# Performance work log

Measured on AMD Instinct MI355X. Metric: run time of the kernel, lower is better.

## Reference

```python
import jax, jax.numpy as jnp
import numpy as np

_DN = ('NCHW', 'OIHW', 'NCHW')

def _conv(x, w, stride=1, pad=1, dil=1, groups=1):
    return jax.lax.conv_general_dilated(
        x, w, window_strides=(stride, stride),
        padding=[(pad, pad), (pad, pad)],
        rhs_dilation=(dil, dil),
        feature_group_count=groups,
        dimension_numbers=_DN)


def setup_inputs() -> dict:
    key = jax.random.key(0)
    k1, k2, k3 = jax.random.split(key, 3)
    B, T, C_in, H, W = 4, 16, 32, 64, 64
    hidden = 64
    x = jax.random.normal(k1, (B, T, C_in, H, W), dtype=jnp.float32)
    # input-to-hidden conv weight: 3 gates stacked along out channels
    fan_i = C_in * 3 * 3
    W_i = jax.random.normal(k2, (3 * hidden, C_in, 3, 3), dtype=jnp.float32) / np.sqrt(fan_i)
    fan_h = hidden * 3 * 3
    W_h = jax.random.normal(k3, (3 * hidden, hidden, 3, 3), dtype=jnp.float32) / np.sqrt(fan_h)
    return {"x": x, "W_i": W_i, "W_h": W_h}


def reference(x, W_i, W_h):
    # x: [B, T, C_in, H, W] (batch_first). Single-layer unidirectional ConvGRU.
    B, T, C_in, H, Wd = x.shape
    hidden = W_h.shape[1]

    def cell(h, x_t):
        gi = _conv(x_t, W_i)          # [B, 3*hidden, H, W]
        gh = _conv(h, W_h)            # [B, 3*hidden, H, W]
        i_r, i_z, i_n = jnp.split(gi, 3, axis=1)
        h_r, h_z, h_n = jnp.split(gh, 3, axis=1)
        r = jax.nn.sigmoid(i_r + h_r)
        z = jax.nn.sigmoid(i_z + h_z)
        n = jnp.tanh(i_n + r * h_n)
        h_new = (1.0 - z) * n + z * h
        return h_new, h_new

    h0 = jnp.zeros((B, hidden, H, Wd), dtype=x.dtype)
    xs = jnp.moveaxis(x, 1, 0)        # [T, B, C_in, H, W]
    _, hs = jax.lax.scan(cell, h0, xs)
    return jnp.moveaxis(hs, 0, 1)     # [B, T, hidden, H, W]
```

## Files before the change

kernel.cpp:

```cpp
#include <hip/hip_runtime.h>
#include <math.h>

constexpr int B_  = 4;
constexpr int T_  = 16;
constexpr int CIN = 32;
constexpr int HID = 64;
constexpr int HH  = 64;
constexpr int WW  = 64;
constexpr int HW  = HH * WW;

constexpr int TR = 8,  TC = 16;
constexpr int PR = TR + 2, PC = TC + 2;
constexpr int CSL = 40;
constexpr int KCH = 32;
constexpr int ASLAB_HW  = 3 * 36 * 16 * 8;
constexpr int ATOTAL    = 12 * ASLAB_HW;
constexpr int TIN_HW    = PR * PC * CSL;
constexpr int TIN_GRAN  = TIN_HW / 8;
constexpr int ROW_HW    = 66 * CSL;
constexpr int PIMG_HW   = 66 * ROW_HW;

constexpr size_t A2_HW    = (size_t)ATOTAL;
constexpr size_t XT_OFF   = A2_HW;
constexpr size_t XT_HW    = (size_t)64 * PIMG_HW;
constexpr size_t HT_OFF   = XT_OFF + XT_HW;
constexpr size_t HTBUF_HW = (size_t)8 * PIMG_HW;
constexpr size_t WS_NEED_BYTES = (A2_HW + XT_HW + 2 * HTBUF_HW) * 2;

typedef __attribute__((ext_vector_type(8))) short bf16x8;
typedef __attribute__((ext_vector_type(4))) float f32x4;

#define GLOAD_LDS16(gsrc, ldst) \
  __builtin_amdgcn_global_load_lds((const __attribute__((address_space(1))) void*)(gsrc), \
                                   (__attribute__((address_space(3))) void*)(ldst), 16, 0, 0)

__device__ inline unsigned short f2bf(float f) {
    union { float f; unsigned u; } v; v.f = f;
    return (unsigned short)((v.u + 0x7FFFu + ((v.u >> 16) & 1u)) >> 16);
}
__device__ inline float bf2f(unsigned short h) {
    union { unsigned u; float f; } v; v.u = (unsigned)h << 16; return v.f;
}

__global__ void wconv(const float* __restrict__ Wi, const float* __restrict__ Wh,
                      unsigned short* __restrict__ A2) {
    int idx = blockIdx.x * 256 + threadIdx.x;
    if (idx >= ATOTAL) return;
    int ic  = idx & 31;
    int r1  = idx >> 5;
    int tap = r1 % 9;
    int r2  = r1 / 9;
    int m   = r2 & 15;
    int r3  = r2 >> 4;
    int gt  = r3 % 3;
    int r4  = r3 / 3;
    int hg  = r4 & 3;
    int ch  = r4 >> 2;
    int o   = gt * 64 + hg * 16 + m;
    float w = (ch == 0) ? Wi[(o * CIN + ic) * 9 + tap]
                        : Wh[(o * HID + (ch - 1) * 32 + ic) * 9 + tap];
    size_t dst = (size_t)(ch * 4 + hg) * ASLAB_HW
               + ((size_t)(gt * 36 + tap * 4 + (ic >> 3)) * 16 + m) * 8 + (ic & 7);
    A2[dst] = f2bf(w);
}

__global__ void xfill(const float* __restrict__ x, unsigned short* __restrict__ xT) {
    const int riT = blockIdx.x;
    const int bt  = blockIdx.y;
    unsigned short* dst = xT + (size_t)bt * PIMG_HW + (size_t)riT * ROW_HW;
    __shared__ float lds[64 * 41];

    const bool interior = (riT >= 1 && riT <= 64);
    if (interior) {
        const float* src = x + (size_t)bt * 32 * HW + (riT - 1) * WW;
        const int p = threadIdx.x & 63;
        #pragma unroll
        for (int j = 0; j < 8; ++j) {
            int c = j * 4 + (threadIdx.x >> 6);
            lds[p * 41 + c] = src[c * HW + p];
        }
    }
    __syncthreads();
    for (int g = threadIdx.x; g < ROW_HW / 8; g += 256) {
        bf16x8 vv;
        #pragma unroll
        for (int k = 0; k < 8; ++k) {
            int off = g * 8 + k;
            int px = off / CSL, slot = off - px * CSL;
            float v = 0.f;
            if (interior && slot < 32 && px >= 1 && px <= 64)
                v = lds[(px - 1) * 41 + slot];
            vv[k] = (short)f2bf(v);
        }
        *(bf16x8*)(dst + g * 8) = vv;
    }
}

__global__ void hzero(unsigned short* __restrict__ hT, int n16) {
    int i = blockIdx.x * 256 + threadIdx.x;
    if (i < n16) ((f32x4*)hT)[i] = f32x4{0.f, 0.f, 0.f, 0.f};
}

__global__ __launch_bounds__(256, 2) void convgru_mfma(
    const unsigned short* __restrict__ xT,
    const unsigned short* __restrict__ A2,
    const unsigned short* __restrict__ hTrd,
    unsigned short* __restrict__ hTwr,
    float* __restrict__ out, int t)
{
    __shared__ __align__(16) unsigned short t0s[TIN_HW];
    __shared__ __align__(16) unsigned short t1s[TIN_HW];
    __shared__ __align__(16) unsigned short t2s[TIN_HW];

    const int tid  = threadIdx.x;
    const int lane = tid & 63, wave = tid >> 6;
    const int px   = lane & 15, kl = lane >> 4;
    const int ty = blockIdx.x >> 2, tx = blockIdx.x & 3;
    const int hg = blockIdx.y, b = blockIdx.z;
    const int gy0 = ty * TR, gx0 = tx * TC;

    const unsigned short* xs = xT + (size_t)(b * T_ + t) * PIMG_HW;
    const int rowbase = gy0 * 66 + gx0;

    f32x4 accR[2] = {}, accZ[2] = {}, accNX[2] = {}, accNH[2] = {};
    bf16x8 a[27];

    auto stage_tin = [&](const unsigned short* src, unsigned short* dst) {
        #pragma unroll
        for (int j = 0; j < 4; ++j) {
            int G = tid + j * 256;
            if (G < TIN_GRAN) {
                int r = G / 90, w = G - 90 * r;
                GLOAD_LDS16(src + (size_t)(rowbase + r * 66) * CSL + w * 8, dst + G * 8);
            }
        }
    };
    auto regA = [&](int ch) {
        const unsigned short* s = A2 + (size_t)(ch * 4 + hg) * ASLAB_HW + lane * 8;
        #pragma unroll
        for (int i = 0; i < 27; ++i)
            a[i] = *(const bf16x8*)(s + (size_t)((i / 9) * 36 + (i % 9) * 4) * 128);
    };

    const int rb = (wave * 2 * PC + px) * CSL + kl * 8;

    auto compute = [&](const unsigned short* tb, bool isX) {
        bf16x8 P[4][3];
        #pragma unroll
        for (int r = 0; r < 4; ++r)
            #pragma unroll
            for (int s = 0; s < 3; ++s)
                P[r][s] = *(const bf16x8*)(tb + rb + (r * PC + s) * CSL);
        #pragma unroll
        for (int dy = 0; dy < 3; ++dy) {
            #pragma unroll
            for (int dx = 0; dx < 3; ++dx) {
                const int tap = dy * 3 + dx;
                bf16x8 b0 = P[dy][dx], b1 = P[dy + 1][dx];
                bf16x8 ar = a[tap], az = a[9 + tap], an = a[18 + tap];
                accR[0] = __builtin_amdgcn_mfma_f32_16x16x32_bf16(ar, b0, accR[0], 0, 0, 0);
                accR[1] = __builtin_amdgcn_mfma_f32_16x16x32_bf16(ar, b1, accR[1], 0, 0, 0);
                accZ[0] = __builtin_amdgcn_mfma_f32_16x16x32_bf16(az, b0, accZ[0], 0, 0, 0);
                accZ[1] = __builtin_amdgcn_mfma_f32_16x16x32_bf16(az, b1, accZ[1], 0, 0, 0);
                if (isX) {
                    accNX[0] = __builtin_amdgcn_mfma_f32_16x16x32_bf16(an, b0, accNX[0], 0, 0, 0);
                    accNX[1] = __builtin_amdgcn_mfma_f32_16x16x32_bf16(an, b1, accNX[1], 0, 0, 0);
                } else {
                    accNH[0] = __builtin_amdgcn_mfma_f32_16x16x32_bf16(an, b0, accNH[0], 0, 0, 0);
                    accNH[1] = __builtin_amdgcn_mfma_f32_16x16x32_bf16(an, b1, accNH[1], 0, 0, 0);
                }
            }
        }
    };

    stage_tin(xs, t0s);
    if (t > 0) {
        stage_tin(hTrd + (size_t)(b * 2 + 0) * PIMG_HW, t1s);
        stage_tin(hTrd + (size_t)(b * 2 + 1) * PIMG_HW, t2s);
    }
    regA(0);
    __syncthreads();
    compute(t0s, true);
    if (t > 0) {
        regA(1);
        compute(t1s, false);
        regA(2);
        compute(t2s, false);
    }

    float* outp = out + ((size_t)(b * T_ + t)) * HID * HW;
    const int c0   = hg * 16 + kl * 4;
    const int slot = c0 & 31;
    const unsigned short* hbuf = (hg < 2) ? t1s : t2s;
    #pragma unroll
    for (int g = 0; g < 2; ++g) {
        int gy = gy0 + wave * 2 + g;
        int gx = gx0 + px;
        float hvf[4] = {0.f, 0.f, 0.f, 0.f};
        if (t > 0) {
            const unsigned short* hp =
                hbuf + ((wave * 2 + g + 1) * PC + (px + 1)) * CSL + slot;
            #pragma unroll
            for (int q = 0; q < 4; ++q) hvf[q] = bf2f(hp[q]);
        }
        unsigned short hvals[4];
        #pragma unroll
        for (int q = 0; q < 4; ++q) {
            int c = c0 + q;
            float sr = __builtin_amdgcn_rcpf(1.f + __expf(-accR[g][q]));
            float sz = __builtin_amdgcn_rcpf(1.f + __expf(-accZ[g][q]));
            float ag = accNX[g][q] + sr * accNH[g][q];
            float nn = 2.f * __builtin_amdgcn_rcpf(1.f + __expf(-2.f * ag)) - 1.f;
            float hn = nn + sz * (hvf[q] - nn);
            outp[(size_t)c * HW + gy * WW + gx] = hn;
            hvals[q] = f2bf(hn);
        }
        unsigned short* hd = hTwr + (size_t)(b * 2 + (c0 >> 5)) * PIMG_HW
                           + (size_t)((gy + 1) * 66 + (gx + 1)) * CSL + slot;
        *(uint2*)hd = *(const uint2*)hvals;
    }
}

constexpr int F_AROWB = 640;
constexpr int R4_ASLAB = 48 * 9 * KCH;
constexpr int R4_AVEC  = R4_ASLAB / 8;
constexpr int R4_ATOT  = 12 * R4_ASLAB;
__global__ void wconv_r4(const float* __restrict__ Wi, const float* __restrict__ Wh,
                         unsigned short* __restrict__ A2) {
    int idx = blockIdx.x * 256 + threadIdx.x;
    if (idx >= R4_ATOT) return;
    int ic = idx & 31; int r1 = idx >> 5;
    int tap = r1 % 9; int r2 = r1 / 9;
    int m = r2 & 15; int r3 = r2 >> 4;
    int gt = r3 % 3; int r4 = r3 / 3;
    int hg = r4 & 3; int ch = r4 >> 2;
    int o = gt * 64 + hg * 16 + m;
    float w = (ch == 0) ? Wi[(o * CIN + ic) * 9 + tap]
                        : Wh[(o * HID + (ch - 1) * 32 + ic) * 9 + tap];
    A2[idx] = f2bf(w);
}
__global__ __launch_bounds__(256, 2) void convgru_r4(
    const float* __restrict__ x, const unsigned short* __restrict__ A2,
    const float* hall, float* out, int t)
{
    __shared__ __align__(16) unsigned short tin[PR * PC * 40];
    __shared__ __align__(16) unsigned short Alr[48 * (F_AROWB / 2)];
    const int tid = threadIdx.x;
    const int lane = tid & 63, wave = tid >> 6;
    const int px = lane & 15, kl = lane >> 4;
    const int ty = blockIdx.x >> 2, tx = blockIdx.x & 3;
    const int hg = blockIdx.y, b = blockIdx.z;
    const int gy0 = ty * TR, gx0 = tx * TC;
    const int nch = (t > 0) ? 3 : 1;
    const float* hb = (t > 0) ? (hall + ((size_t)(b * T_ + t - 1)) * HID * HW) : nullptr;
    const float* xb = x + ((size_t)(b * T_ + t)) * CIN * HW;
    f32x4 accR[2] = {}, accZ[2] = {}, accNX[2] = {}, accNH[2] = {};
    float ireg[23]; bf16x8 areg[7];
    auto load_in = [&](int ch) {
        const float* src = (ch == 0) ? xb : (hb + (size_t)(ch - 1) * KCH * HW);
        #pragma unroll
        for (int j = 0; j < 23; ++j) {
            int e = tid + j * 256; float v = 0.f;
            if (e < PR * PC * KCH) {
                int ic = e / (PR * PC); int rem = e - ic * (PR * PC);
                int r = rem / PC, c = rem - r * PC;
                int gy = gy0 + r - 1, gx = gx0 + c - 1;
                if ((unsigned)gy < (unsigned)HH && (unsigned)gx < (unsigned)WW)
                    v = src[ic * HW + gy * WW + gx];
            }
            ireg[j] = v;
        }
    };
    auto load_Ar = [&](int ch) {
        const unsigned short* s = A2 + (size_t)(ch * 4 + hg) * R4_ASLAB;
        #pragma unroll
        for (int j = 0; j < 7; ++j) { int v = tid + j * 256; if (v < R4_AVEC) areg[j] = *(const bf16x8*)(s + v * 8); }
    };
    auto write_in = [&]() {
        #pragma unroll
        for (int j = 0; j < 23; ++j) {
            int e = tid + j * 256;
            if (e < PR * PC * KCH) {
                int ic = e / (PR * PC); int rem = e - ic * (PR * PC);
                int r = rem / PC, c = rem - r * PC;
                tin[(r * PC + c) * 40 + ic] = f2bf(ireg[j]);
            }
        }
    };
    auto write_Ar = [&]() {
        #pragma unroll
        for (int j = 0; j < 7; ++j) {
            int v = tid + j * 256;
            if (v < R4_AVEC) {
                int row = v / 36; int kb = (v - row * 36) * 16;
                char* dst = (char*)Alr + row * F_AROWB + (kb ^ ((row & 7) << 4));
                *(bf16x8*)dst = areg[j];
            }
        }
    };
    const int rb0 = ((wave * 2 + 0) * PC + px) * 40 + kl * 8;
    const int rb1 = rb0 + PC * 40;
    const int swA = (px & 7) << 4;
    auto compute = [&](bool isX) {
        #pragma unroll
        for (int tap = 0; tap < 9; ++tap) {
            const int dy = tap / 3, dx = tap - 3 * dy;
            const int toff = (dy * PC + dx) * 40;
            bf16x8 b0 = *(const bf16x8*)(tin + rb0 + toff);
            bf16x8 b1 = *(const bf16x8*)(tin + rb1 + toff);
            const char* ab = (const char*)Alr + px * F_AROWB + ((tap * 64 + kl * 16) ^ swA);
            bf16x8 ar = *(const bf16x8*)(ab);
            bf16x8 az = *(const bf16x8*)(ab + 16 * F_AROWB);
            bf16x8 an = *(const bf16x8*)(ab + 32 * F_AROWB);
            accR[0] = __builtin_amdgcn_mfma_f32_16x16x32_bf16(ar, b0, accR[0], 0, 0, 0);
            accR[1] = __builtin_amdgcn_mfma_f32_16x16x32_bf16(ar, b1, accR[1], 0, 0, 0);
            accZ[0] = __builtin_amdgcn_mfma_f32_16x16x32_bf16(az, b0, accZ[0], 0, 0, 0);
            accZ[1] = __builtin_amdgcn_mfma_f32_16x16x32_bf16(az, b1, accZ[1], 0, 0, 0);
            if (isX) {
                accNX[0] = __builtin_amdgcn_mfma_f32_16x16x32_bf16(an, b0, accNX[0], 0, 0, 0);
                accNX[1] = __builtin_amdgcn_mfma_f32_16x16x32_bf16(an, b1, accNX[1], 0, 0, 0);
            } else {
                accNH[0] = __builtin_amdgcn_mfma_f32_16x16x32_bf16(an, b0, accNH[0], 0, 0, 0);
                accNH[1] = __builtin_amdgcn_mfma_f32_16x16x32_bf16(an, b1, accNH[1], 0, 0, 0);
            }
        }
    };
    load_in(0); load_Ar(0); write_in(); write_Ar();
    __syncthreads();
    for (int ch = 0; ch < nch; ++ch) {
        if (ch + 1 < nch) { load_in(ch + 1); load_Ar(ch + 1); }
        compute(ch == 0);
        __syncthreads();
        if (ch + 1 < nch) { write_in(); write_Ar(); __syncthreads(); }
    }
    float* outp = out + ((size_t)(b * T_ + t)) * HID * HW;
    #pragma unroll
    for (int g = 0; g < 2; ++g) {
        int gy = gy0 + wave * 2 + g; int gx = gx0 + px;
        #pragma unroll
        for (int q = 0; q < 4; ++q) {
            int c = hg * 16 + kl * 4 + q;
            float sr = 1.f / (1.f + expf(-accR[g][q]));
            float sz = 1.f / (1.f + expf(-accZ[g][q]));
            float nn = tanhf(accNX[g][q] + sr * accNH[g][q]);
            float hv = hb ? hb[(size_t)c * HW + gy * WW + gx] : 0.f;
            outp[(size_t)c * HW + gy * WW + gx] = (1.f - sz) * nn + sz * hv;
        }
    }
}

extern "C" void kernel_launch(void* const* d_in, const int* in_sizes, int n_in,
                              void* d_out, int out_size, void* d_ws, size_t ws_size,
                              hipStream_t stream) {
    const float* x  = (const float*)d_in[0];
    const float* Wi = (const float*)d_in[1];
    const float* Wh = (const float*)d_in[2];
    float* out = (float*)d_out;

    if (ws_size >= WS_NEED_BYTES) {
        unsigned short* A2  = (unsigned short*)d_ws;
        unsigned short* xT  = A2 + XT_OFF;
        unsigned short* hT0 = A2 + HT_OFF;
        unsigned short* hT1 = hT0 + HTBUF_HW;

        wconv<<<(ATOTAL + 255) / 256, 256, 0, stream>>>(Wi, Wh, A2);
        xfill<<<dim3(66, 64), 256, 0, stream>>>(x, xT);
        {
            int n16 = (int)(2 * HTBUF_HW / 8);
            hzero<<<(n16 + 255) / 256, 256, 0, stream>>>(hT0, n16);
        }
        for (int t = 0; t < T_; ++t) {
            unsigned short* rd = (t & 1) ? hT1 : hT0;
            unsigned short* wr = (t & 1) ? hT0 : hT1;
            convgru_mfma<<<dim3(32, 4, 4), 256, 0, stream>>>(xT, A2, rd, wr, out, t);
        }
    } else {
        unsigned short* A2 = (unsigned short*)d_ws;
        wconv_r4<<<(R4_ATOT + 255) / 256, 256, 0, stream>>>(Wi, Wh, A2);
        for (int t = 0; t < T_; ++t)
            convgru_r4<<<dim3(32, 4, 4), 256, 0, stream>>>(x, A2, out, out, t);
    }
}
```

Before: 174.5 us.

## Merge prep kernels into one launch and prefetch next-channel weights during MFMA

Combines the weight conversion, x repacking and hidden-state zeroing into a single prep kernel that dispatches on block index, removing two kernel launches. Inside the recurrent kernel, the weight registers for the next channel chunk are loaded tap by tap while the current chunk's MFMAs run, instead of a blocking reload between chunks. This hides global weight-load latency but reuses the same register array in place, which could raise register pressure or limit how freely the compiler schedules the loads.

```diff
diff --git a/kernel.cpp b/kernel.cpp
--- a/kernel.cpp
+++ b/kernel.cpp
@@ -27,6 +27,12 @@
 constexpr size_t HTBUF_HW = (size_t)8 * PIMG_HW;
 constexpr size_t WS_NEED_BYTES = (A2_HW + XT_HW + 2 * HTBUF_HW) * 2;
 
+constexpr int PB_XFILL = 66 * 64;
+constexpr int PB_WCONV = (ATOTAL + 255) / 256;
+constexpr int HZ_GRAN  = (int)(2 * HTBUF_HW / 8);
+constexpr int PB_HZERO = (HZ_GRAN + 255) / 256;
+constexpr int PB_TOTAL = PB_XFILL + PB_WCONV + PB_HZERO;
+
 typedef __attribute__((ext_vector_type(8))) short bf16x8;
 typedef __attribute__((ext_vector_type(4))) float f32x4;
 
@@ -42,63 +48,65 @@
     union { unsigned u; float f; } v; v.u = (unsigned)h << 16; return v.f;
 }
 
-__global__ void wconv(const float* __restrict__ Wi, const float* __restrict__ Wh,
-                      unsigned short* __restrict__ A2) {
-    int idx = blockIdx.x * 256 + threadIdx.x;
-    if (idx >= ATOTAL) return;
-    int ic  = idx & 31;
-    int r1  = idx >> 5;
-    int tap = r1 % 9;
-    int r2  = r1 / 9;
-    int m   = r2 & 15;
-    int r3  = r2 >> 4;
-    int gt  = r3 % 3;
-    int r4  = r3 / 3;
-    int hg  = r4 & 3;
-    int ch  = r4 >> 2;
-    int o   = gt * 64 + hg * 16 + m;
-    float w = (ch == 0) ? Wi[(o * CIN + ic) * 9 + tap]
-                        : Wh[(o * HID + (ch - 1) * 32 + ic) * 9 + tap];
-    size_t dst = (size_t)(ch * 4 + hg) * ASLAB_HW
-               + ((size_t)(gt * 36 + tap * 4 + (ic >> 3)) * 16 + m) * 8 + (ic & 7);
-    A2[dst] = f2bf(w);
-}
-
-__global__ void xfill(const float* __restrict__ x, unsigned short* __restrict__ xT) {
-    const int riT = blockIdx.x;
-    const int bt  = blockIdx.y;
-    unsigned short* dst = xT + (size_t)bt * PIMG_HW + (size_t)riT * ROW_HW;
+__global__ void prep(const float* __restrict__ x,
+                     const float* __restrict__ Wi, const float* __restrict__ Wh,
+                     unsigned short* __restrict__ A2,
+                     unsigned short* __restrict__ xT,
+                     unsigned short* __restrict__ hT) {
     __shared__ float lds[64 * 41];
-
-    const bool interior = (riT >= 1 && riT <= 64);
-    if (interior) {
-        const float* src = x + (size_t)bt * 32 * HW + (riT - 1) * WW;
-        const int p = threadIdx.x & 63;
-        #pragma unroll
-        for (int j = 0; j < 8; ++j) {
-            int c = j * 4 + (threadIdx.x >> 6);
-            lds[p * 41 + c] = src[c * HW + p];
-        }
-    }
-    __syncthreads();
-    for (int g = threadIdx.x; g < ROW_HW / 8; g += 256) {
-        bf16x8 vv;
-        #pragma unroll
-        for (int k = 0; k < 8; ++k) {
-            int off = g * 8 + k;
-            int px = off / CSL, slot = off - px * CSL;
-            float v = 0.f;
-            if (interior && slot < 32 && px >= 1 && px <= 64)
-                v = lds[(px - 1) * 41 + slot];
-            vv[k] = (short)f2bf(v);
-        }
-        *(bf16x8*)(dst + g * 8) = vv;
-    }
-}
-
-__global__ void hzero(unsigned short* __restrict__ hT, int n16) {
-    int i = blockIdx.x * 256 + threadIdx.x;
-    if (i < n16) ((f32x4*)hT)[i] = f32x4{0.f, 0.f, 0.f, 0.f};
+    const int bid = blockIdx.x;
+
+    if (bid < PB_XFILL) {
+        const int riT = bid % 66;
+        const int bt  = bid / 66;
+        unsigned short* dst = xT + (size_t)bt * PIMG_HW + (size_t)riT * ROW_HW;
+        const bool interior = (riT >= 1 && riT <= 64);
+        if (interior) {
+            const float* src = x + (size_t)bt * 32 * HW + (riT - 1) * WW;
+            const int p = threadIdx.x & 63;
+            #pragma unroll
+            for (int j = 0; j < 8; ++j) {
+                int c = j * 4 + (threadIdx.x >> 6);
+                lds[p * 41 + c] = src[c * HW + p];
+            }
+        }
+        __syncthreads();
+        for (int g = threadIdx.x; g < ROW_HW / 8; g += 256) {
+            bf16x8 vv;
+            #pragma unroll
+            for (int k = 0; k < 8; ++k) {
+                int off = g * 8 + k;
+                int px = off / CSL, slot = off - px * CSL;
+                float v = 0.f;
+                if (interior && slot < 32 && px >= 1 && px <= 64)
+                    v = lds[(px - 1) * 41 + slot];
+                vv[k] = (short)f2bf(v);
+            }
+            *(bf16x8*)(dst + g * 8) = vv;
+        }
+    } else if (bid < PB_XFILL + PB_WCONV) {
+        int idx = (bid - PB_XFILL) * 256 + threadIdx.x;
+        if (idx >= ATOTAL) return;
+        int ic  = idx & 31;
+        int r1  = idx >> 5;
+        int tap = r1 % 9;
+        int r2  = r1 / 9;
+        int m   = r2 & 15;
+        int r3  = r2 >> 4;
+        int gt  = r3 % 3;
+        int r4  = r3 / 3;
+        int hg  = r4 & 3;
+        int ch  = r4 >> 2;
+        int o   = gt * 64 + hg * 16 + m;
+        float w = (ch == 0) ? Wi[(o * CIN + ic) * 9 + tap]
+                            : Wh[(o * HID + (ch - 1) * 32 + ic) * 9 + tap];
+        size_t dst = (size_t)(ch * 4 + hg) * ASLAB_HW
+                   + ((size_t)(gt * 36 + tap * 4 + (ic >> 3)) * 16 + m) * 8 + (ic & 7);
+        A2[dst] = f2bf(w);
+    } else {
+        int i = (bid - PB_XFILL - PB_WCONV) * 256 + threadIdx.x;
+        if (i < HZ_GRAN) ((f32x4*)hT)[i] = f32x4{0.f, 0.f, 0.f, 0.f};
+    }
 }
 
 __global__ __launch_bounds__(256, 2) void convgru_mfma(
@@ -144,7 +152,7 @@
 
     const int rb = (wave * 2 * PC + px) * CSL + kl * 8;
 
-    auto compute = [&](const unsigned short* tb, bool isX) {
+    auto compute = [&](const unsigned short* tb, bool isX, const unsigned short* nextA) {
         bf16x8 P[4][3];
         #pragma unroll
         for (int r = 0; r < 4; ++r)
@@ -158,6 +166,11 @@
                 const int tap = dy * 3 + dx;
                 bf16x8 b0 = P[dy][dx], b1 = P[dy + 1][dx];
                 bf16x8 ar = a[tap], az = a[9 + tap], an = a[18 + tap];
+                if (nextA) {
+                    a[tap]      = *(const bf16x8*)(nextA + (size_t)(0 * 36 + tap * 4) * 128);
+                    a[9 + tap]  = *(const bf16x8*)(nextA + (size_t)(1 * 36 + tap * 4) * 128);
+                    a[18 + tap] = *(const bf16x8*)(nextA + (size_t)(2 * 36 + tap * 4) * 128);
+                }
                 accR[0] = __builtin_amdgcn_mfma_f32_16x16x32_bf16(ar, b0, accR[0], 0, 0, 0);
                 accR[1] = __builtin_amdgcn_mfma_f32_16x16x32_bf16(ar, b1, accR[1], 0, 0, 0);
                 accZ[0] = __builtin_amdgcn_mfma_f32_16x16x32_bf16(az, b0, accZ[0], 0, 0, 0);
@@ -180,12 +193,16 @@
     }
     regA(0);
     __syncthreads();
-    compute(t0s, true);
+
+    const unsigned short* A1p = (t > 0)
+        ? A2 + (size_t)(1 * 4 + hg) * ASLAB_HW + lane * 8 : nullptr;
+    const unsigned short* A2p = (t > 0)
+        ? A2 + (size_t)(2 * 4 + hg) * ASLAB_HW + lane * 8 : nullptr;
+
+    compute(t0s, true, A1p);
     if (t > 0) {
-        regA(1);
-        compute(t1s, false);
-        regA(2);
-        compute(t2s, false);
+        compute(t1s, false, A2p);
+        compute(t2s, false, nullptr);
     }
 
     float* outp = out + ((size_t)(b * T_ + t)) * HID * HW;
@@ -363,12 +380,7 @@
         unsigned short* hT0 = A2 + HT_OFF;
         unsigned short* hT1 = hT0 + HTBUF_HW;
 
-        wconv<<<(ATOTAL + 255) / 256, 256, 0, stream>>>(Wi, Wh, A2);
-        xfill<<<dim3(66, 64), 256, 0, stream>>>(x, xT);
-        {
-            int n16 = (int)(2 * HTBUF_HW / 8);
-            hzero<<<(n16 + 255) / 256, 256, 0, stream>>>(hT0, n16);
-        }
+        prep<<<PB_TOTAL, 256, 0, stream>>>(x, Wi, Wh, A2, xT, hT0);
         for (int t = 0; t < T_; ++t) {
             unsigned short* rd = (t & 1) ? hT1 : hT0;
             unsigned short* wr = (t & 1) ? hT0 : hT1;
```

After: 166.7 us. -4.5%, faster.
